# Kernel optimization log

Hardware: AMD Instinct MI355X
Metric: run time of the kernel (lower is better)

The kernel has to match this reference:

```python
import jax, jax.numpy as jnp
import numpy as np

B, D, K = 8, 128, 7          # batch, num objects, per-object feature
Q = 256                      # question embedding size
G0, G1 = 511, 512            # g-layer sizes
F1, F2, OUT = 512, 1024, 16  # f-layer sizes


def setup_inputs() -> dict:
    key = jax.random.key(0)
    ks = jax.random.split(key, 14)
    def lin(kw, kb, fan_in, fan_out):
        lim = 1.0 / np.sqrt(fan_in)
        w = jax.random.uniform(kw, (fan_in, fan_out), jnp.float32, -lim, lim)
        b = jax.random.uniform(kb, (fan_out,), jnp.float32, -lim, lim)
        return w, b
    x = jax.random.normal(ks[0], (B, D, K), jnp.float32)
    qst = jax.random.normal(ks[1], (B, Q), jnp.float32)
    g0_w, g0_b = lin(ks[2], ks[3], 2 * K, G0)
    g1_w, g1_b = lin(ks[4], ks[5], G0 + Q, G1)
    f1_w, f1_b = lin(ks[6], ks[7], G1, F1)
    f2_w, f2_b = lin(ks[8], ks[9], F1, F2)
    f3_w, f3_b = lin(ks[10], ks[11], F2, OUT)
    return {"x": x, "qst": qst,
            "g0_w": g0_w, "g0_b": g0_b, "g1_w": g1_w, "g1_b": g1_b,
            "f1_w": f1_w, "f1_b": f1_b, "f2_w": f2_w, "f2_b": f2_b,
            "f3_w": f3_w, "f3_b": f3_b}


def reference(x, qst, g0_w, g0_b, g1_w, g1_b, f1_w, f1_b, f2_w, f2_b, f3_w, f3_b):
    b, d, k = x.shape
    # all-pairs: torch x_i[b,a,c,:]=x[b,c,:], x_j[b,a,c,:]=x[b,a,:]
    x_i = jnp.broadcast_to(x[:, None, :, :], (b, d, d, k))
    x_j = jnp.broadcast_to(x[:, :, None, :], (b, d, d, k))
    pairs = jnp.concatenate([x_i, x_j], axis=-1)            # (b,d,d,2k)
    h = jax.nn.relu(pairs @ g0_w + g0_b)                    # (b,d,d,G0)
    q = jnp.broadcast_to(qst[:, None, None, :], (b, d, d, qst.shape[-1]))
    h = jnp.concatenate([h, q], axis=-1)                    # (b,d,d,G0+Q)
    h = jax.nn.relu(h @ g1_w + g1_b)                        # (b,d,d,G1)
    x_g = h.sum(axis=(1, 2))                                # sum over d^2 pairs -> (b,G1)
    f = jax.nn.relu(x_g @ f1_w + f1_b)
    f = jax.nn.relu(f @ f2_w + f2_b)                        # dropout = identity (eval)
    logits = f @ f3_w + f3_b
    return jax.nn.log_softmax(logits, axis=1)
```

## Files before the change

### kernel.cpp

```cpp
#include <hip/hip_runtime.h>
#include <hip/hip_bf16.h>

#define B_  8
#define D_  128
#define K_  7
#define Q_  256
#define G0_ 511
#define G0P 512
#define G1_ 512
#define F1_ 512
#define F2_ 1024
#define OUT_ 16

typedef __bf16 bf16x8 __attribute__((ext_vector_type(8)));
typedef float  f32x4  __attribute__((ext_vector_type(4)));

#define GL2LDS(g, l) __builtin_amdgcn_global_load_lds(                        \
    (const __attribute__((address_space(1))) void*)(g),                       \
    (__attribute__((address_space(3))) void*)(l), 16, 0, 0)

__global__ void k_prep(const float* __restrict__ x, const float* __restrict__ g0w,
                       const float* __restrict__ g0b, const float* __restrict__ qst,
                       const float* __restrict__ g1w, const float* __restrict__ g1b,
                       const float* __restrict__ f1w, const float* __restrict__ f2w,
                       const float* __restrict__ f3w,
                       float* __restrict__ u, float* __restrict__ v,
                       __bf16* __restrict__ w1t, float* __restrict__ qterm,
                       float* __restrict__ xg, float* __restrict__ f1t,
                       float* __restrict__ f2t, float* __restrict__ f3t) {
    const int blk = blockIdx.x;
    const int t   = threadIdx.x;
    if (blk < 1024) {
        __shared__ float xs[8];
        if (t < K_) xs[t] = x[blk * K_ + t];
        __syncthreads();
        #pragma unroll
        for (int h = 0; h < 2; ++h) {
            const int g = t + h * 256;
            float su = 0.f, sv = 0.f;
            if (g < G0_) {
                #pragma unroll
                for (int k = 0; k < K_; ++k) {
                    su += xs[k] * g0w[k * G0_ + g];
                    sv += xs[k] * g0w[(K_ + k) * G0_ + g];
                }
                su += g0b[g];
            }
            u[blk * G0P + g] = (g < G0_) ? su : 0.f;
            v[blk * G0P + g] = (g < G0_) ? sv : 0.f;
        }
    } else if (blk < 1280) {
        __shared__ __bf16 tile[32][33];
        const int bb = blk - 1024;
        const int bx = bb & 15, by = bb >> 4;
        const int r = t >> 5, c = t & 31;
        #pragma unroll
        for (int i = 0; i < 4; ++i) {
            const int k = by * 32 + r + i * 8;
            const int n = bx * 32 + c;
            tile[r + i * 8][c] = (__bf16)((k < G0_) ? g1w[k * G1_ + n] : 0.f);
        }
        __syncthreads();
        #pragma unroll
        for (int i = 0; i < 4; ++i) {
            const int n = bx * 32 + r + i * 8;
            const int cc = (c >> 3) & 3, j = c & 7;
            const int slot = cc ^ ((n >> 1) & 3);
            w1t[by * 16384 + n * 32 + slot * 8 + j] = tile[c][r + i * 8];
        }
    } else if (blk < 1312) {
        __shared__ float qs[256];
        __shared__ float red[2][128];
        const int qb = blk - 1280;
        const int b = qb >> 2, nb = (qb & 3) << 7;
        qs[t] = qst[b * Q_ + t];
        __syncthreads();
        const int n = nb + (t & 127);
        const int qh = (t >> 7) * 128;
        float s = 0.f;
        #pragma unroll 8
        for (int q = 0; q < 128; ++q)
            s += qs[qh + q] * g1w[(G0_ + qh + q) * G1_ + n];
        red[t >> 7][t & 127] = s;
        __syncthreads();
        if (t < 128)
            qterm[b * G1_ + nb + t] = red[0][t] + red[1][t] + g1b[nb + t];
    } else if (blk < 1320) {
        const int b = blk - 1312;
        xg[b * G1_ + t] = 0.f;
        xg[b * G1_ + 256 + t] = 0.f;
    } else if (blk < 1576) {
        __shared__ float tile[32][33];
        const int j = blk - 1320;
        const int bo = j & 15, bk = j >> 4;
        const int r = t >> 5, c = t & 31;
        #pragma unroll
        for (int i = 0; i < 4; ++i)
            tile[r + i * 8][c] = f1w[(bk * 32 + r + i * 8) * F1_ + bo * 32 + c];
        __syncthreads();
        #pragma unroll
        for (int i = 0; i < 4; ++i)
            f1t[(bo * 32 + r + i * 8) * G1_ + bk * 32 + c] = tile[c][r + i * 8];
    } else if (blk < 2088) {
        __shared__ float tile[32][33];
        const int j = blk - 1576;
        const int bo = j & 31, bk = j >> 5;
        const int r = t >> 5, c = t & 31;
        #pragma unroll
        for (int i = 0; i < 4; ++i)
            tile[r + i * 8][c] = f2w[(bk * 32 + r + i * 8) * F2_ + bo * 32 + c];
        __syncthreads();
        #pragma unroll
        for (int i = 0; i < 4; ++i)
            f2t[(bo * 32 + r + i * 8) * F1_ + bk * 32 + c] = tile[c][r + i * 8];
    } else {
        const int k = (blk - 2088) * 256 + t;
        float4 r0 = *(const float4*)(f3w + k * OUT_);
        float4 r1 = *(const float4*)(f3w + k * OUT_ + 4);
        float4 r2 = *(const float4*)(f3w + k * OUT_ + 8);
        float4 r3 = *(const float4*)(f3w + k * OUT_ + 12);
        const float rr[16] = {r0.x,r0.y,r0.z,r0.w, r1.x,r1.y,r1.z,r1.w,
                              r2.x,r2.y,r2.z,r2.w, r3.x,r3.y,r3.z,r3.w};
        #pragma unroll
        for (int o = 0; o < 16; ++o) f3t[o * F2_ + k] = rr[o];
    }
}

__global__ __launch_bounds__(512, 4)
void k_pair(const float* __restrict__ u, const float* __restrict__ v,
            const __bf16* __restrict__ w1t, const float* __restrict__ qterm,
            float* __restrict__ xg) {
    __shared__ float  v_a[512];
    __shared__ __bf16 At[2][4096];
    __shared__ __bf16 Bt[3][8192];
    __shared__ float  ebuf[8][64];

    const int bid  = blockIdx.x;
    const int b    = bid >> 8;
    const int a    = (bid >> 1) & 127;
    const int nbase = (bid & 1) << 8;
    const int tid  = threadIdx.x;
    const int wave = tid >> 6, lane = tid & 63;
    const int quad = lane >> 4, l15 = lane & 15;
    const int wm   = wave >> 2;
    const int wn   = wave & 3;
    const int nloc = wn * 64;
    const int mtg  = wm * 4;
    const int swz  = (l15 >> 1) & 3;

    const int iw0 = wave * 2;
    const __bf16* gsrc = w1t + (size_t)(nbase + iw0 * 16 + (lane >> 2)) * 32
                             + (lane & 3) * 8;

    const int sm = tid >> 2;
    const int q8 = tid & 3;
    const float* urow = u + (size_t)(b * D_ + sm) * G0P + q8 * 8;
    const int woff = ((sm >> 4) * 512 + q8 * 128 + (sm & 15) * 8)
                   ^ (((q8 << 1) | ((sm >> 3) & 1)) << 3);
    const int afoff = (lane ^ (lane >> 3)) * 8;

    f32x4 acc[4][4];
    #pragma unroll
    for (int mt = 0; mt < 4; ++mt)
        #pragma unroll
        for (int nt = 0; nt < 4; ++nt)
            acc[mt][nt] = (f32x4){0.f, 0.f, 0.f, 0.f};

    float4 ua, ub;
    auto load_u = [&](int kq) {
        const float* p = urow + kq * 32;
        ua = *(const float4*)p;
        ub = *(const float4*)(p + 4);
    };
    auto stage_B = [&](int buf, int kq) {
        const __bf16* g = gsrc + (size_t)kq * 16384;
        __bf16* l = &Bt[buf][iw0 * 512];
        GL2LDS(g, l);
        GL2LDS(g + 512, l + 512);
    };
    auto write_A = [&](int buf, int kq) {
        const float* vp = v_a + kq * 32 + q8 * 8;
        const float4 va = *(const float4*)vp;
        const float4 vb = *(const float4*)(vp + 4);
        bf16x8 h;
        h[0] = (__bf16)fmaxf(ua.x + va.x, 0.f);
        h[1] = (__bf16)fmaxf(ua.y + va.y, 0.f);
        h[2] = (__bf16)fmaxf(ua.z + va.z, 0.f);
        h[3] = (__bf16)fmaxf(ua.w + va.w, 0.f);
        h[4] = (__bf16)fmaxf(ub.x + vb.x, 0.f);
        h[5] = (__bf16)fmaxf(ub.y + vb.y, 0.f);
        h[6] = (__bf16)fmaxf(ub.z + vb.z, 0.f);
        h[7] = (__bf16)fmaxf(ub.w + vb.w, 0.f);
        *(bf16x8*)&At[buf][woff] = h;
    };

    float4 vq;
    if (tid < 128) vq = *(const float4*)(v + (b * D_ + a) * G0P + tid * 4);
    load_u(0);
    asm volatile("" ::: "memory");
    stage_B(0, 0);
    stage_B(1, 1);
    if (tid < 128) *(float4*)(v_a + tid * 4) = vq;
    asm volatile("s_waitcnt lgkmcnt(0)\n\ts_barrier" ::: "memory");
    write_A(0, 0);
    asm volatile("s_waitcnt vmcnt(2) lgkmcnt(0)\n\ts_barrier" ::: "memory");

    int bcur = 0, bnxt = 1, bstg = 2;
    for (int kq = 0; kq < 16; ++kq) {
        const int abuf = kq & 1;
        if (kq < 15) load_u(kq + 1);
        asm volatile("" ::: "memory");
        if (kq < 14) stage_B(bstg, kq + 2);

        bf16x8 af[4];
        const __bf16* atb = &At[abuf][mtg * 512 + afoff];
        #pragma unroll
        for (int mt = 0; mt < 4; ++mt)
            af[mt] = *(const bf16x8*)(atb + mt * 512);
        bf16x8 bfr[4];
        const __bf16* btb = &Bt[bcur][(nloc + l15) * 32 + ((quad ^ swz) << 3)];
        #pragma unroll
        for (int nt = 0; nt < 4; ++nt)
            bfr[nt] = *(const bf16x8*)(btb + nt * 512);
        #pragma unroll
        for (int mt = 0; mt < 4; ++mt)
            #pragma unroll
            for (int nt = 0; nt < 4; ++nt)
                acc[mt][nt] = __builtin_amdgcn_mfma_f32_16x16x32_bf16(
                    af[mt], bfr[nt], acc[mt][nt], 0, 0, 0);

        if (kq < 15) write_A(abuf ^ 1, kq + 1);
        asm volatile("s_waitcnt lgkmcnt(0)\n\ts_barrier" ::: "memory");
        const int t3 = bcur; bcur = bnxt; bnxt = bstg; bstg = t3;
    }

    #pragma unroll
    for (int nt = 0; nt < 4; ++nt) {
        const float q = qterm[b * G1_ + nbase + nloc + nt * 16 + l15];
        float s = 0.f;
        #pragma unroll
        for (int mt = 0; mt < 4; ++mt)
            #pragma unroll
            for (int r = 0; r < 4; ++r)
                s += fmaxf(acc[mt][nt][r] + q, 0.f);
        s += __shfl_xor(s, 16, 64);
        s += __shfl_xor(s, 32, 64);
        if (quad == 0) ebuf[wave][nt * 16 + l15] = s;
    }
    __syncthreads();
    if (tid < 256) {
        const float sv = ebuf[tid >> 6][tid & 63] + ebuf[4 + (tid >> 6)][tid & 63];
        atomicAdd(xg + b * G1_ + nbase + tid, sv);
    }
}

__global__ void k_f1(const float* __restrict__ xg, const float* __restrict__ f1t,
                     const float* __restrict__ f1b, float* __restrict__ s1g) {
    const int wave = threadIdx.x >> 6, lane = threadIdx.x & 63;
    const int id = blockIdx.x * 4 + wave;
    const int b = id >> 9, oo = id & 511;
    const float* xr = xg + b * G1_ + lane * 8;
    const float* wr = f1t + oo * G1_ + lane * 8;
    const float4 a0 = *(const float4*)xr, a1 = *(const float4*)(xr + 4);
    const float4 b0 = *(const float4*)wr, b1 = *(const float4*)(wr + 4);
    float s = a0.x*b0.x + a0.y*b0.y + a0.z*b0.z + a0.w*b0.w
            + a1.x*b1.x + a1.y*b1.y + a1.z*b1.z + a1.w*b1.w;
    #pragma unroll
    for (int off = 32; off >= 1; off >>= 1) s += __shfl_xor(s, off, 64);
    if (lane == 0) s1g[b * F1_ + oo] = fmaxf(s + f1b[oo], 0.f);
}

__global__ void k_f2(const float* __restrict__ s1g, const float* __restrict__ f2t,
                     const float* __restrict__ f2b, float* __restrict__ s2g) {
    const int wave = threadIdx.x >> 6, lane = threadIdx.x & 63;
    const int id = blockIdx.x * 4 + wave;
    const int b = id >> 10, oo = id & 1023;
    const float* xr = s1g + b * F1_ + lane * 8;
    const float* wr = f2t + oo * F1_ + lane * 8;
    const float4 a0 = *(const float4*)xr, a1 = *(const float4*)(xr + 4);
    const float4 b0 = *(const float4*)wr, b1 = *(const float4*)(wr + 4);
    float s = a0.x*b0.x + a0.y*b0.y + a0.z*b0.z + a0.w*b0.w
            + a1.x*b1.x + a1.y*b1.y + a1.z*b1.z + a1.w*b1.w;
    #pragma unroll
    for (int off = 32; off >= 1; off >>= 1) s += __shfl_xor(s, off, 64);
    if (lane == 0) s2g[b * F2_ + oo] = fmaxf(s + f2b[oo], 0.f);
}

__global__ void k_f3(const float* __restrict__ s2g, const float* __restrict__ f3t,
                     const float* __restrict__ f3b, float* __restrict__ out) {
    const int b = blockIdx.x, t = threadIdx.x;
    const int wave = t >> 6, lane = t & 63;
    __shared__ float lg[16];
    float4 xs[4];
    #pragma unroll
    for (int j = 0; j < 4; ++j)
        xs[j] = *(const float4*)(s2g + b * F2_ + lane * 16 + j * 4);
    #pragma unroll
    for (int oi = 0; oi < 4; ++oi) {
        const int o = wave * 4 + oi;
        const float* wr = f3t + o * F2_ + lane * 16;
        float s = 0.f;
        #pragma unroll
        for (int j = 0; j < 4; ++j) {
            const float4 w = *(const float4*)(wr + j * 4);
            s += xs[j].x*w.x + xs[j].y*w.y + xs[j].z*w.z + xs[j].w*w.w;
        }
        #pragma unroll
        for (int off = 32; off >= 1; off >>= 1) s += __shfl_xor(s, off, 64);
        if (lane == 0) lg[o] = s + f3b[o];
    }
    __syncthreads();
    if (t < 16) {
        float m = -1e30f;
        #pragma unroll
        for (int i = 0; i < 16; ++i) m = fmaxf(m, lg[i]);
        float se = 0.f;
        #pragma unroll
        for (int i = 0; i < 16; ++i) se += __expf(lg[i] - m);
        out[b * OUT_ + t] = lg[t] - m - logf(se);
    }
}

extern "C" void kernel_launch(void* const* d_in, const int* in_sizes, int n_in,
                              void* d_out, int out_size, void* d_ws, size_t ws_size,
                              hipStream_t stream) {
    const float* x   = (const float*)d_in[0];
    const float* qst = (const float*)d_in[1];
    const float* g0w = (const float*)d_in[2];
    const float* g0b = (const float*)d_in[3];
    const float* g1w = (const float*)d_in[4];
    const float* g1b = (const float*)d_in[5];
    const float* f1w = (const float*)d_in[6];
    const float* f1b = (const float*)d_in[7];
    const float* f2w = (const float*)d_in[8];
    const float* f2b = (const float*)d_in[9];
    const float* f3w = (const float*)d_in[10];
    const float* f3b = (const float*)d_in[11];

    char* ws = (char*)d_ws;
    float*  u     = (float*)ws;  ws += (size_t)B_ * D_ * G0P * 4;
    float*  v     = (float*)ws;  ws += (size_t)B_ * D_ * G0P * 4;
    __bf16* w1t   = (__bf16*)ws; ws += (size_t)G1_ * G0P * 2;
    float*  qterm = (float*)ws;  ws += (size_t)B_ * G1_ * 4;
    float*  xg    = (float*)ws;  ws += (size_t)B_ * G1_ * 4;
    float*  s1g   = (float*)ws;  ws += (size_t)B_ * F1_ * 4;
    float*  s2g   = (float*)ws;  ws += (size_t)B_ * F2_ * 4;
    float*  f1t   = (float*)ws;  ws += (size_t)F1_ * G1_ * 4;
    float*  f2t   = (float*)ws;  ws += (size_t)F2_ * F1_ * 4;
    float*  f3t   = (float*)ws;  ws += (size_t)OUT_ * F2_ * 4;

    k_prep<<<2092, 256, 0, stream>>>(x, g0w, g0b, qst, g1w, g1b, f1w, f2w, f3w,
                                     u, v, w1t, qterm, xg, f1t, f2t, f3t);
    k_pair<<<B_ * D_ * 2, 512, 0, stream>>>(u, v, w1t, qterm, xg);
    k_f1  <<<1024, 256, 0, stream>>>(xg, f1t, f1b, s1g);
    k_f2  <<<2048, 256, 0, stream>>>(s1g, f2t, f2b, s2g);
    k_f3  <<<B_, 256, 0, stream>>>(s2g, f3t, f3b, (float*)d_out);
}
```

Before: 172.2 us.

## Fuse f-layer MLP into one kernel and drop weight transposes

Replaces the separate f1/f2/f3 kernels with a single per-batch kernel of 1024 threads that reads the original row-major weights with coalesced column access. This removes the transpose work in the prep kernel and two kernel launches. It also raises wave priority around the MFMA block in the pair kernel. The fused kernel uses only 8 blocks, so the f2 weight stream is spread over far fewer CUs, which risks a long serial tail.

```diff
diff --git a/kernel.cpp b/kernel.cpp
--- a/kernel.cpp
+++ b/kernel.cpp
@@ -22,12 +22,9 @@
 __global__ void k_prep(const float* __restrict__ x, const float* __restrict__ g0w,
                        const float* __restrict__ g0b, const float* __restrict__ qst,
                        const float* __restrict__ g1w, const float* __restrict__ g1b,
-                       const float* __restrict__ f1w, const float* __restrict__ f2w,
-                       const float* __restrict__ f3w,
                        float* __restrict__ u, float* __restrict__ v,
                        __bf16* __restrict__ w1t, float* __restrict__ qterm,
-                       float* __restrict__ xg, float* __restrict__ f1t,
-                       float* __restrict__ f2t, float* __restrict__ f3t) {
+                       float* __restrict__ xg) {
     const int blk = blockIdx.x;
     const int t   = threadIdx.x;
     if (blk < 1024) {
@@ -85,44 +82,10 @@
         __syncthreads();
         if (t < 128)
             qterm[b * G1_ + nb + t] = red[0][t] + red[1][t] + g1b[nb + t];
-    } else if (blk < 1320) {
+    } else {
         const int b = blk - 1312;
         xg[b * G1_ + t] = 0.f;
         xg[b * G1_ + 256 + t] = 0.f;
-    } else if (blk < 1576) {
-        __shared__ float tile[32][33];
-        const int j = blk - 1320;
-        const int bo = j & 15, bk = j >> 4;
-        const int r = t >> 5, c = t & 31;
-        #pragma unroll
-        for (int i = 0; i < 4; ++i)
-            tile[r + i * 8][c] = f1w[(bk * 32 + r + i * 8) * F1_ + bo * 32 + c];
-        __syncthreads();
-        #pragma unroll
-        for (int i = 0; i < 4; ++i)
-            f1t[(bo * 32 + r + i * 8) * G1_ + bk * 32 + c] = tile[c][r + i * 8];
-    } else if (blk < 2088) {
-        __shared__ float tile[32][33];
-        const int j = blk - 1576;
-        const int bo = j & 31, bk = j >> 5;
-        const int r = t >> 5, c = t & 31;
-        #pragma unroll
-        for (int i = 0; i < 4; ++i)
-            tile[r + i * 8][c] = f2w[(bk * 32 + r + i * 8) * F2_ + bo * 32 + c];
-        __syncthreads();
-        #pragma unroll
-        for (int i = 0; i < 4; ++i)
-            f2t[(bo * 32 + r + i * 8) * F1_ + bk * 32 + c] = tile[c][r + i * 8];
-    } else {
-        const int k = (blk - 2088) * 256 + t;
-        float4 r0 = *(const float4*)(f3w + k * OUT_);
-        float4 r1 = *(const float4*)(f3w + k * OUT_ + 4);
-        float4 r2 = *(const float4*)(f3w + k * OUT_ + 8);
-        float4 r3 = *(const float4*)(f3w + k * OUT_ + 12);
-        const float rr[16] = {r0.x,r0.y,r0.z,r0.w, r1.x,r1.y,r1.z,r1.w,
-                              r2.x,r2.y,r2.z,r2.w, r3.x,r3.y,r3.z,r3.w};
-        #pragma unroll
-        for (int o = 0; o < 16; ++o) f3t[o * F2_ + k] = rr[o];
     }
 }
 
@@ -222,12 +185,14 @@
         #pragma unroll
         for (int nt = 0; nt < 4; ++nt)
             bfr[nt] = *(const bf16x8*)(btb + nt * 512);
+        __builtin_amdgcn_s_setprio(1);
         #pragma unroll
         for (int mt = 0; mt < 4; ++mt)
             #pragma unroll
             for (int nt = 0; nt < 4; ++nt)
                 acc[mt][nt] = __builtin_amdgcn_mfma_f32_16x16x32_bf16(
                     af[mt], bfr[nt], acc[mt][nt], 0, 0, 0);
+        __builtin_amdgcn_s_setprio(0);
 
         if (kq < 15) write_A(abuf ^ 1, kq + 1);
         asm volatile("s_waitcnt lgkmcnt(0)\n\ts_barrier" ::: "memory");
@@ -254,70 +219,62 @@
     }
 }
 
-__global__ void k_f1(const float* __restrict__ xg, const float* __restrict__ f1t,
-                     const float* __restrict__ f1b, float* __restrict__ s1g) {
-    const int wave = threadIdx.x >> 6, lane = threadIdx.x & 63;
-    const int id = blockIdx.x * 4 + wave;
-    const int b = id >> 9, oo = id & 511;
-    const float* xr = xg + b * G1_ + lane * 8;
-    const float* wr = f1t + oo * G1_ + lane * 8;
-    const float4 a0 = *(const float4*)xr, a1 = *(const float4*)(xr + 4);
-    const float4 b0 = *(const float4*)wr, b1 = *(const float4*)(wr + 4);
-    float s = a0.x*b0.x + a0.y*b0.y + a0.z*b0.z + a0.w*b0.w
-            + a1.x*b1.x + a1.y*b1.y + a1.z*b1.z + a1.w*b1.w;
-    #pragma unroll
-    for (int off = 32; off >= 1; off >>= 1) s += __shfl_xor(s, off, 64);
-    if (lane == 0) s1g[b * F1_ + oo] = fmaxf(s + f1b[oo], 0.f);
-}
-
-__global__ void k_f2(const float* __restrict__ s1g, const float* __restrict__ f2t,
-                     const float* __restrict__ f2b, float* __restrict__ s2g) {
-    const int wave = threadIdx.x >> 6, lane = threadIdx.x & 63;
-    const int id = blockIdx.x * 4 + wave;
-    const int b = id >> 10, oo = id & 1023;
-    const float* xr = s1g + b * F1_ + lane * 8;
-    const float* wr = f2t + oo * F1_ + lane * 8;
-    const float4 a0 = *(const float4*)xr, a1 = *(const float4*)(xr + 4);
-    const float4 b0 = *(const float4*)wr, b1 = *(const float4*)(wr + 4);
-    float s = a0.x*b0.x + a0.y*b0.y + a0.z*b0.z + a0.w*b0.w
-            + a1.x*b1.x + a1.y*b1.y + a1.z*b1.z + a1.w*b1.w;
-    #pragma unroll
-    for (int off = 32; off >= 1; off >>= 1) s += __shfl_xor(s, off, 64);
-    if (lane == 0) s2g[b * F2_ + oo] = fmaxf(s + f2b[oo], 0.f);
-}
-
-__global__ void k_f3(const float* __restrict__ s2g, const float* __restrict__ f3t,
-                     const float* __restrict__ f3b, float* __restrict__ out) {
-    const int b = blockIdx.x, t = threadIdx.x;
-    const int wave = t >> 6, lane = t & 63;
+__global__ __launch_bounds__(1024)
+void k_f(const float* __restrict__ xg,
+         const float* __restrict__ f1w, const float* __restrict__ f1b,
+         const float* __restrict__ f2w, const float* __restrict__ f2b,
+         const float* __restrict__ f3w, const float* __restrict__ f3b,
+         float* __restrict__ out) {
+    const int b = blockIdx.x, tid = threadIdx.x;
+    __shared__ float xs[512];
+    __shared__ float s1[512];
+    __shared__ float s2[1024];
+    __shared__ float red[1024];
     __shared__ float lg[16];
-    float4 xs[4];
-    #pragma unroll
-    for (int j = 0; j < 4; ++j)
-        xs[j] = *(const float4*)(s2g + b * F2_ + lane * 16 + j * 4);
-    #pragma unroll
-    for (int oi = 0; oi < 4; ++oi) {
-        const int o = wave * 4 + oi;
-        const float* wr = f3t + o * F2_ + lane * 16;
+    if (tid < 512) xs[tid] = xg[b * G1_ + tid];
+    __syncthreads();
+    {
+        const int o = tid & 511, h = tid >> 9;
+        const float* w = f1w + (size_t)(h * 256) * F1_ + o;
+        float acc = 0.f;
+        #pragma unroll 8
+        for (int k = 0; k < 256; ++k)
+            acc += xs[h * 256 + k] * w[(size_t)k * F1_];
+        red[tid] = acc;
+    }
+    __syncthreads();
+    if (tid < 512) s1[tid] = fmaxf(red[tid] + red[tid + 512] + f1b[tid], 0.f);
+    __syncthreads();
+    {
+        const float* w = f2w + tid;
+        float acc = 0.f;
+        #pragma unroll 8
+        for (int k = 0; k < 512; ++k)
+            acc += s1[k] * w[(size_t)k * F2_];
+        s2[tid] = fmaxf(acc + f2b[tid], 0.f);
+    }
+    __syncthreads();
+    {
+        const int wv = tid >> 6, lane = tid & 63;
         float s = 0.f;
         #pragma unroll
-        for (int j = 0; j < 4; ++j) {
-            const float4 w = *(const float4*)(wr + j * 4);
-            s += xs[j].x*w.x + xs[j].y*w.y + xs[j].z*w.z + xs[j].w*w.w;
+        for (int j = 0; j < 16; ++j) {
+            const int k = j * 64 + lane;
+            s += s2[k] * f3w[k * OUT_ + wv];
         }
         #pragma unroll
         for (int off = 32; off >= 1; off >>= 1) s += __shfl_xor(s, off, 64);
-        if (lane == 0) lg[o] = s + f3b[o];
-    }
-    __syncthreads();
-    if (t < 16) {
+        if (lane == 0) lg[wv] = s + f3b[wv];
+    }
+    __syncthreads();
+    if (tid < 16) {
         float m = -1e30f;
         #pragma unroll
         for (int i = 0; i < 16; ++i) m = fmaxf(m, lg[i]);
         float se = 0.f;
         #pragma unroll
         for (int i = 0; i < 16; ++i) se += __expf(lg[i] - m);
-        out[b * OUT_ + t] = lg[t] - m - logf(se);
+        out[b * OUT_ + tid] = lg[tid] - m - logf(se);
     }
 }
 
@@ -343,16 +300,10 @@
     __bf16* w1t   = (__bf16*)ws; ws += (size_t)G1_ * G0P * 2;
     float*  qterm = (float*)ws;  ws += (size_t)B_ * G1_ * 4;
     float*  xg    = (float*)ws;  ws += (size_t)B_ * G1_ * 4;
-    float*  s1g   = (float*)ws;  ws += (size_t)B_ * F1_ * 4;
-    float*  s2g   = (float*)ws;  ws += (size_t)B_ * F2_ * 4;
-    float*  f1t   = (float*)ws;  ws += (size_t)F1_ * G1_ * 4;
-    float*  f2t   = (float*)ws;  ws += (size_t)F2_ * F1_ * 4;
-    float*  f3t   = (float*)ws;  ws += (size_t)OUT_ * F2_ * 4;
-
-    k_prep<<<2092, 256, 0, stream>>>(x, g0w, g0b, qst, g1w, g1b, f1w, f2w, f3w,
-                                     u, v, w1t, qterm, xg, f1t, f2t, f3t);
+
+    k_prep<<<1320, 256, 0, stream>>>(x, g0w, g0b, qst, g1w, g1b,
+                                     u, v, w1t, qterm, xg);
     k_pair<<<B_ * D_ * 2, 512, 0, stream>>>(u, v, w1t, qterm, xg);
-    k_f1  <<<1024, 256, 0, stream>>>(xg, f1t, f1b, s1g);
-    k_f2  <<<2048, 256, 0, stream>>>(s1g, f2t, f2b, s2g);
-    k_f3  <<<B_, 256, 0, stream>>>(s2g, f3t, f3b, (float*)d_out);
+    k_f   <<<B_, 1024, 0, stream>>>(xg, f1w, f1b, f2w, f2b, f3w, f3b,
+                                    (float*)d_out);
 }
```

Result: slower. 208.9 us (+21.3%).
